# Performance work log

Hardware: AMD Instinct MI355X
Metric: run time of the kernel (lower is better)

The kernel has to match this reference:

```python
import jax, jax.numpy as jnp
import numpy as np

B, C, H, W = 32, 1536, 32, 32
M_CLUSTERS, L_DIM, G_DIM = 64, 128, 256
SINKHORN_ITERS = 3
EPS = 1e-12

def setup_inputs() -> dict:
    key = jax.random.key(0)
    ks = jax.random.split(key, 16)
    s = lambda i, shape, scale=0.02: jax.random.normal(ks[i], shape, jnp.float32) * scale
    return {
        'x': jax.random.normal(ks[0], (B, C, H, W), jnp.float32),
        't': jax.random.normal(ks[1], (B, C), jnp.float32),
        'cf_w1': s(2, (512, C)), 'cf_b1': s(3, (512,)),
        'cf_w2': s(4, (L_DIM, 512)), 'cf_b2': s(5, (L_DIM,)),
        'sc_w1': s(6, (512, C)), 'sc_b1': s(7, (512,)),
        'sc_w2': s(8, (M_CLUSTERS, 512)), 'sc_b2': s(9, (M_CLUSTERS,)),
        'tk_w1': s(10, (512, C)), 'tk_b1': s(11, (512,)),
        'tk_w2': s(12, (G_DIM, 512)), 'tk_b2': s(13, (G_DIM,)),
        'dust_bin': jnp.array(1.0, jnp.float32),
    }

def _l2norm(v, axis):
    n = jnp.sqrt(jnp.sum(v * v, axis=axis, keepdims=True))
    return v / jnp.maximum(n, EPS)

def _log_optimal_transport(scores, alpha, iters):
    # scores: [B, m, n]; append dustbin row, run log-space Sinkhorn
    b, m, n = scores.shape
    norm = -jnp.log(jnp.float32(m + n))
    bins = jnp.broadcast_to(alpha, (b, 1, n))
    Z0 = jnp.concatenate([scores, bins], axis=1)             # [B, m+1, n]
    log_mu = jnp.concatenate([jnp.full((m,), norm, jnp.float32),
                              jnp.log(jnp.float32(n - m))[None] + norm])  # [m+1]
    log_nu = jnp.full((n,), norm, jnp.float32)               # [n]
    u = jnp.zeros((b, m + 1), jnp.float32)
    v = jnp.zeros((b, n), jnp.float32)
    for _ in range(iters):
        u = log_mu[None, :] - jax.nn.logsumexp(Z0 + v[:, None, :], axis=2)
        v = log_nu[None, :] - jax.nn.logsumexp(Z0 + u[:, :, None], axis=1)
    return Z0 + u[:, :, None] + v[:, None, :] - norm

def reference(x, t, cf_w1, cf_b1, cf_w2, cf_b2, sc_w1, sc_b1, sc_w2, sc_b2,
              tk_w1, tk_b1, tk_w2, tk_b2, dust_bin):
    b = x.shape[0]
    xf = x.reshape(b, x.shape[1], -1)                        # [B, C, HW]
    # cluster_features: 1x1 conv stack -> [B, l, HW]
    h = jax.nn.relu(jnp.einsum('oc,bcn->bon', cf_w1, xf) + cf_b1[None, :, None])
    f = jnp.einsum('oc,bcn->bon', cf_w2, h) + cf_b2[None, :, None]
    # score: 1x1 conv stack -> [B, m, HW]
    h = jax.nn.relu(jnp.einsum('oc,bcn->bon', sc_w1, xf) + sc_b1[None, :, None])
    p = jnp.einsum('oc,bcn->bon', sc_w2, h) + sc_b2[None, :, None]
    # token_features: MLP -> [B, g]
    tk = jax.nn.relu(t @ tk_w1.T + tk_b1) @ tk_w2.T + tk_b2
    # Sinkhorn OT assignment, drop dustbin row
    p = jnp.exp(_log_optimal_transport(p, dust_bin, SINKHORN_ITERS))[:, :-1, :]  # [B, m, HW]
    # fused VLAD aggregation (avoids the repeat-materialized tensors)
    agg = jnp.einsum('bln,bmn->blm', f, p)                   # [B, l, m]
    agg = _l2norm(agg, axis=1).reshape(b, -1)                # [B, l*m]
    v = jnp.concatenate([_l2norm(tk, axis=-1), agg], axis=-1)
    return _l2norm(v, axis=-1)
```

## Files before the change

### kernel.cpp

```cpp
#include <hip/hip_runtime.h>
#include <hip/hip_bf16.h>
#include <math.h>

typedef unsigned short u16;
typedef __attribute__((ext_vector_type(8))) short short8;
typedef __attribute__((ext_vector_type(4))) float floatx4;

#define DEVINL __device__ __forceinline__

DEVINL float bf2f(u16 u) { union { unsigned int i; float f; } v; v.i = ((unsigned int)u) << 16; return v.f; }
DEVINL u16 f2bf(float f) {
  union { unsigned int i; float f; } v; v.f = f;
  unsigned int i = v.i;
  unsigned int r = (i + 0x7fffu + ((i >> 16) & 1u)) >> 16;
  return (u16)r;
}

__global__ __launch_bounds__(256) void k_prep(
    const float* __restrict__ cf_w1, u16* __restrict__ wc1,
    const float* __restrict__ sc_w1, u16* __restrict__ ws1,
    const float* __restrict__ cf_w2, u16* __restrict__ wc2,
    const float* __restrict__ sc_w2, u16* __restrict__ ws2p,
    const float* __restrict__ sc_b2, float* __restrict__ scb2p) {
  int i = blockIdx.x * 256 + threadIdx.x;
  int job = blockIdx.y;
  if (job == 4) {
    if (i < 128) scb2p[i] = (i < 64) ? sc_b2[i] : 0.f;
    return;
  }
  const float* src = (job == 0) ? cf_w1 : (job == 1) ? sc_w1 : (job == 2) ? cf_w2 : sc_w2;
  u16* dst = (job == 0) ? wc1 : (job == 1) ? ws1 : (job == 2) ? wc2 : ws2p;
  int n4 = (job <= 1) ? 196608 : 16384;
  if (i >= n4) return;
  ushort4 o = {0, 0, 0, 0};
  if (job != 3 || (i >> 7) < 64) {
    float4 v = ((const float4*)src)[i];
    o.x = f2bf(v.x); o.y = f2bf(v.y); o.z = f2bf(v.z); o.w = f2bf(v.w);
  }
  ((ushort4*)dst)[i] = o;
}

__global__ __launch_bounds__(256) void k_transpose(const float* __restrict__ x,
                                                   u16* __restrict__ xT,
                                                   int nC, int nN) {
  __shared__ u16 tile[64 * 65];
  int b = blockIdx.z;
  int c0 = blockIdx.y * 64, n0 = blockIdx.x * 64;
  const float* xb = x + ((long)b * nC + c0) * nN + n0;
  u16* xTb = xT + ((long)b * nN + n0) * nC + c0;
  int tid = threadIdx.x;
#pragma unroll
  for (int p = 0; p < 2; ++p) {
    int u = tid + p * 256;
    int r = u >> 3, nc = (u & 7) * 8;
    const float4* srcp = (const float4*)(xb + (long)r * nN + nc);
    float4 v0 = srcp[0], v1 = srcp[1];
    int base = r * 65 + nc;
    tile[base + 0] = f2bf(v0.x); tile[base + 1] = f2bf(v0.y);
    tile[base + 2] = f2bf(v0.z); tile[base + 3] = f2bf(v0.w);
    tile[base + 4] = f2bf(v1.x); tile[base + 5] = f2bf(v1.y);
    tile[base + 6] = f2bf(v1.z); tile[base + 7] = f2bf(v1.w);
  }
  __syncthreads();
#pragma unroll
  for (int p = 0; p < 2; ++p) {
    int u = tid + p * 256;
    int nr = u >> 3, cc = (u & 7) * 8;
    __align__(16) u16 tmp[8];
#pragma unroll
    for (int j = 0; j < 8; ++j) tmp[j] = tile[(cc + j) * 65 + nr];
    *(uint4*)(xTb + (long)nr * nC + cc) = *(uint4*)(tmp);
  }
}

template <bool OUT_F32, int BIAS_MODE, bool RELU>
__global__ __launch_bounds__(256) void k_gemm64(
    const u16* __restrict__ A, int lda, long aBS,
    const u16* __restrict__ B1, const u16* __restrict__ B2, int nSplit,
    int ldb, long bBS,
    void* __restrict__ Out, int ldo, long oBS,
    const float* __restrict__ bias1, const float* __restrict__ bias2,
    int M, int N, int K) {
  __shared__ __align__(16) u16 As[128 * 64];
  __shared__ __align__(16) u16 Bs[128 * 64];
  int bz = blockIdx.z;
  int m0 = blockIdx.x * 128, n0 = blockIdx.y * 128;
  const u16* Ablk = A + (long)bz * aBS + (long)m0 * lda;
  const u16* Bblk =
      ((n0 < nSplit) ? (B1 + (long)n0 * ldb) : (B2 + (long)(n0 - nSplit) * ldb)) +
      (long)bz * bBS;
  int tid = threadIdx.x;
  int lane = tid & 63;
  int lane16 = lane & 15, quad = lane >> 4;
  int wid = tid >> 6;
  int wm = wid >> 1, wn = wid & 1;

  int rIn = lane >> 3;
  int kkSw = ((lane & 7) ^ rIn) * 8;

  floatx4 acc[4][4];
#pragma unroll
  for (int i = 0; i < 4; ++i)
#pragma unroll
    for (int j = 0; j < 4; ++j) acc[i][j] = (floatx4){0.f, 0.f, 0.f, 0.f};

  for (int k0 = 0; k0 < K; k0 += 64) {
    __syncthreads();
#pragma unroll
    for (int h = 0; h < 4; ++h) {
      int ch = wid * 4 + h;
      int r = ch * 8 + rIn;
      const u16* srcA = Ablk + (long)r * lda + k0 + kkSw;
      __builtin_amdgcn_global_load_lds(
          (const __attribute__((address_space(1))) void*)srcA,
          (__attribute__((address_space(3))) void*)&As[ch * 512], 16, 0, 0);
      const u16* srcB = Bblk + (long)r * ldb + k0 + kkSw;
      __builtin_amdgcn_global_load_lds(
          (const __attribute__((address_space(1))) void*)srcB,
          (__attribute__((address_space(3))) void*)&Bs[ch * 512], 16, 0, 0);
    }
    __syncthreads();
#pragma unroll
    for (int h2 = 0; h2 < 2; ++h2) {
      short8 af[4], bfr[4];
#pragma unroll
      for (int t = 0; t < 4; ++t) {
        int ra = wm * 64 + t * 16 + lane16;
        af[t] = *(const short8*)&As[ra * 64 + (((h2 * 4 + quad) ^ (ra & 7)) * 8)];
      }
#pragma unroll
      for (int t = 0; t < 4; ++t) {
        int rb = wn * 64 + t * 16 + lane16;
        bfr[t] = *(const short8*)&Bs[rb * 64 + (((h2 * 4 + quad) ^ (rb & 7)) * 8)];
      }
#pragma unroll
      for (int i = 0; i < 4; ++i)
#pragma unroll
        for (int j = 0; j < 4; ++j)
          acc[i][j] = __builtin_amdgcn_mfma_f32_16x16x32_bf16(af[i], bfr[j],
                                                              acc[i][j], 0, 0, 0);
    }
  }

  const float* bcolPtr = bias1;
  int bofs = 0;
  if (BIAS_MODE == 2 && n0 >= nSplit) { bcolPtr = bias2; bofs = nSplit; }
#pragma unroll
  for (int i = 0; i < 4; ++i) {
    int rowb = m0 + wm * 64 + i * 16 + quad * 4;
#pragma unroll
    for (int j = 0; j < 4; ++j) {
      int col = n0 + wn * 64 + j * 16 + lane16;
      float bc = 0.f;
      if (BIAS_MODE == 2) bc = bcolPtr[col - bofs];
#pragma unroll
      for (int r = 0; r < 4; ++r) {
        int row = rowb + r;
        float v = acc[i][j][r];
        if (BIAS_MODE == 2) v += bc;
        if (BIAS_MODE == 1) v += bias1[row];
        if (RELU) v = fmaxf(v, 0.f);
        if (OUT_F32)
          ((float*)Out)[(long)bz * oBS + (long)row * ldo + col] = v;
        else
          ((u16*)Out)[(long)bz * oBS + (long)row * ldo + col] = f2bf(v);
      }
    }
  }
}

__global__ __launch_bounds__(256) void k_k2dual(
    const u16* __restrict__ wA, const u16* __restrict__ wB,
    const u16* __restrict__ hT, u16* __restrict__ fOut, u16* __restrict__ sOut,
    const float* __restrict__ bA, const float* __restrict__ bB) {
  __shared__ __align__(16) u16 As[128 * 64];
  __shared__ __align__(16) u16 Bs[128 * 64];
  int sel = blockIdx.y, bz = blockIdx.z;
  const u16* A = sel ? wB : wA;
  const u16* Bbase = hT + (long)bz * 1048576 + (sel ? 512 : 0);
  u16* Out = (sel ? sOut : fOut) + (long)bz * 131072;
  const float* bias = sel ? bB : bA;
  int n0 = blockIdx.x * 128;
  int tid = threadIdx.x;
  int lane = tid & 63;
  int lane16 = lane & 15, quad = lane >> 4;
  int wid = tid >> 6;
  int wm = wid >> 1, wn = wid & 1;
  int rIn = lane >> 3;
  int kkSw = ((lane & 7) ^ rIn) * 8;

  floatx4 acc[4][4];
#pragma unroll
  for (int i = 0; i < 4; ++i)
#pragma unroll
    for (int j = 0; j < 4; ++j) acc[i][j] = (floatx4){0.f, 0.f, 0.f, 0.f};

  for (int k0 = 0; k0 < 512; k0 += 64) {
    __syncthreads();
#pragma unroll
    for (int h = 0; h < 4; ++h) {
      int ch = wid * 4 + h;
      int r = ch * 8 + rIn;
      const u16* srcA = A + (long)r * 512 + k0 + kkSw;
      __builtin_amdgcn_global_load_lds(
          (const __attribute__((address_space(1))) void*)srcA,
          (__attribute__((address_space(3))) void*)&As[ch * 512], 16, 0, 0);
      const u16* srcB = Bbase + (long)(n0 + r) * 1024 + k0 + kkSw;
      __builtin_amdgcn_global_load_lds(
          (const __attribute__((address_space(1))) void*)srcB,
          (__attribute__((address_space(3))) void*)&Bs[ch * 512], 16, 0, 0);
    }
    __syncthreads();
#pragma unroll
    for (int h2 = 0; h2 < 2; ++h2) {
      short8 af[4], bfr[4];
#pragma unroll
      for (int t = 0; t < 4; ++t) {
        int ra = wm * 64 + t * 16 + lane16;
        af[t] = *(const short8*)&As[ra * 64 + (((h2 * 4 + quad) ^ (ra & 7)) * 8)];
      }
#pragma unroll
      for (int t = 0; t < 4; ++t) {
        int rb = wn * 64 + t * 16 + lane16;
        bfr[t] = *(const short8*)&Bs[rb * 64 + (((h2 * 4 + quad) ^ (rb & 7)) * 8)];
      }
#pragma unroll
      for (int i = 0; i < 4; ++i)
#pragma unroll
        for (int j = 0; j < 4; ++j)
          acc[i][j] = __builtin_amdgcn_mfma_f32_16x16x32_bf16(af[i], bfr[j],
                                                              acc[i][j], 0, 0, 0);
    }
  }
#pragma unroll
  for (int i = 0; i < 4; ++i) {
    int rowb = wm * 64 + i * 16 + quad * 4;
#pragma unroll
    for (int j = 0; j < 4; ++j) {
      int col = n0 + wn * 64 + j * 16 + lane16;
#pragma unroll
      for (int r = 0; r < 4; ++r) {
        int row = rowb + r;
        Out[(long)row * 1024 + col] = f2bf(acc[i][j][r] + bias[row]);
      }
    }
  }
}

__global__ __launch_bounds__(1024) void k_sinkhorn(
    const u16* __restrict__ S, const float* __restrict__ alphaPtr,
    float lmu, float lmu_bin, float lnu, float norm, u16* __restrict__ P) {
  __shared__ float u_[65];
  __shared__ float v_[1024];
  int b = blockIdx.x, tid = threadIdx.x;
  const u16* Sb = S + (long)b * 131072;
  float alpha = *alphaPtr;
  v_[tid] = 0.f;
  __syncthreads();
  int wid = tid >> 6, lane = tid & 63;
  for (int it = 0; it < 3; ++it) {
    for (int i = wid; i < 65; i += 16) {
      float vals[16];
      float mx = -3.4e38f;
#pragma unroll
      for (int s = 0; s < 16; ++s) {
        int j = lane + s * 64;
        float z = (i < 64 ? bf2f(Sb[i * 1024 + j]) : alpha) + v_[j];
        vals[s] = z;
        mx = fmaxf(mx, z);
      }
#pragma unroll
      for (int off = 32; off > 0; off >>= 1) mx = fmaxf(mx, __shfl_xor(mx, off));
      float sum = 0.f;
#pragma unroll
      for (int s = 0; s < 16; ++s) sum += __expf(vals[s] - mx);
#pragma unroll
      for (int off = 32; off > 0; off >>= 1) sum += __shfl_xor(sum, off);
      if (lane == 0) u_[i] = (i < 64 ? lmu : lmu_bin) - (mx + __logf(sum));
    }
    __syncthreads();
    {
      float mx = alpha + u_[64];
#pragma unroll 8
      for (int i = 0; i < 64; ++i)
        mx = fmaxf(mx, bf2f(Sb[i * 1024 + tid]) + u_[i]);
      float sum = __expf(alpha + u_[64] - mx);
#pragma unroll 8
      for (int i = 0; i < 64; ++i)
        sum += __expf(bf2f(Sb[i * 1024 + tid]) + u_[i] - mx);
      v_[tid] = lnu - (mx + __logf(sum));
    }
    __syncthreads();
  }
  float vj = v_[tid];
  u16* Pb = P + (long)b * 65536;
#pragma unroll 8
  for (int i = 0; i < 64; ++i) {
    float z = bf2f(Sb[i * 1024 + tid]) + u_[i] + vj - norm;
    Pb[i * 1024 + tid] = f2bf(__expf(fminf(z, 1.0f)));
  }
}

__global__ __launch_bounds__(256) void k_agg(const u16* __restrict__ f,
                                             const u16* __restrict__ P,
                                             float* __restrict__ aggP) {
  __shared__ __align__(16) u16 Fs[128 * 32];
  __shared__ __align__(16) u16 Ps[64 * 32];
  int bz = blockIdx.z, kc = blockIdx.x;
  const u16* Fb = f + (long)bz * 128 * 1024;
  const u16* Pb = P + (long)bz * 64 * 1024;
  int tid = threadIdx.x, wid = tid >> 6, lane = tid & 63;
  int lane16 = lane & 15, quad = lane >> 4;
  int rA0 = lane >> 2, kk = (lane & 3) * 8;

  floatx4 acc[2][4];
#pragma unroll
  for (int i = 0; i < 2; ++i)
#pragma unroll
    for (int j = 0; j < 4; ++j) acc[i][j] = (floatx4){0.f, 0.f, 0.f, 0.f};

  for (int k0 = kc * 256; k0 < kc * 256 + 256; k0 += 32) {
    __syncthreads();
#pragma unroll
    for (int h = 0; h < 2; ++h) {
      int ch = wid * 2 + h;
      int r = ch * 16 + rA0;
      const u16* srcF = Fb + (long)r * 1024 + k0 + kk;
      __builtin_amdgcn_global_load_lds(
          (const __attribute__((address_space(1))) void*)srcF,
          (__attribute__((address_space(3))) void*)&Fs[ch * 512], 16, 0, 0);
    }
    {
      int r = wid * 16 + rA0;
      const u16* srcP = Pb + (long)r * 1024 + k0 + kk;
      __builtin_amdgcn_global_load_lds(
          (const __attribute__((address_space(1))) void*)srcP,
          (__attribute__((address_space(3))) void*)&Ps[wid * 512], 16, 0, 0);
    }
    __syncthreads();
    short8 af[2], bfr[4];
#pragma unroll
    for (int t = 0; t < 2; ++t)
      af[t] = *(const short8*)&Fs[(wid * 32 + t * 16 + lane16) * 32 + quad * 8];
#pragma unroll
    for (int j = 0; j < 4; ++j)
      bfr[j] = *(const short8*)&Ps[(j * 16 + lane16) * 32 + quad * 8];
#pragma unroll
    for (int i = 0; i < 2; ++i)
#pragma unroll
      for (int j = 0; j < 4; ++j)
        acc[i][j] = __builtin_amdgcn_mfma_f32_16x16x32_bf16(af[i], bfr[j],
                                                            acc[i][j], 0, 0, 0);
  }
  float* ab = aggP + ((long)kc * 32 + bz) * 8192;
#pragma unroll
  for (int i = 0; i < 2; ++i)
#pragma unroll
    for (int j = 0; j < 4; ++j)
#pragma unroll
      for (int r = 0; r < 4; ++r) {
        int row = wid * 32 + i * 16 + quad * 4 + r;
        int col = j * 16 + lane16;
        ab[row * 64 + col] = acc[i][j][r];
      }
}

DEVINL float waveSum(float x) {
#pragma unroll
  for (int off = 32; off > 0; off >>= 1) x += __shfl_xor(x, off);
  return x;
}

__global__ __launch_bounds__(256) void k_mlp1(const float* __restrict__ t,
                                              const float* __restrict__ w1,
                                              const float* __restrict__ b1,
                                              float* __restrict__ h1) {
  __shared__ float tl[1536];
  int b = blockIdx.y, og = blockIdx.x;
  int tid = threadIdx.x, wid = tid >> 6, lane = tid & 63;
  for (int i = tid; i < 1536; i += 256) tl[i] = t[b * 1536 + i];
  __syncthreads();
#pragma unroll 4
  for (int oi = 0; oi < 16; ++oi) {
    int o = og * 64 + wid * 16 + oi;
    const float* wr = w1 + (long)o * 1536;
    float acc = 0.f;
#pragma unroll
    for (int s = 0; s < 24; ++s) { int c = lane + s * 64; acc += tl[c] * wr[c]; }
    acc = waveSum(acc);
    if (lane == 0) h1[b * 512 + o] = fmaxf(acc + b1[o], 0.f);
  }
}

__global__ __launch_bounds__(256) void k_mlp2(const float* __restrict__ h1,
                                              const float* __restrict__ w2,
                                              const float* __restrict__ b2,
                                              float* __restrict__ tk) {
  __shared__ float hl[512];
  int b = blockIdx.y, og = blockIdx.x;
  int tid = threadIdx.x, wid = tid >> 6, lane = tid & 63;
  for (int i = tid; i < 512; i += 256) hl[i] = h1[b * 512 + i];
  __syncthreads();
#pragma unroll 4
  for (int oi = 0; oi < 16; ++oi) {
    int o = og * 64 + wid * 16 + oi;
    const float* wr = w2 + (long)o * 512;
    float acc = 0.f;
#pragma unroll
    for (int s = 0; s < 8; ++s) { int c = lane + s * 64; acc += hl[c] * wr[c]; }
    acc = waveSum(acc);
    if (lane == 0) tk[b * 256 + o] = acc + b2[o];
  }
}

DEVINL float blockSum256(float x, float* red) {
#pragma unroll
  for (int off = 32; off > 0; off >>= 1) x += __shfl_xor(x, off);
  int wid = threadIdx.x >> 6;
  __syncthreads();
  if ((threadIdx.x & 63) == 0) red[wid] = x;
  __syncthreads();
  return red[0] + red[1] + red[2] + red[3];
}

__global__ __launch_bounds__(256) void k_norms(const float* __restrict__ tk,
                                               const float* __restrict__ aggP,
                                               float* __restrict__ out) {
  __shared__ float asum[8192];
  __shared__ float cn[64];
  __shared__ float red[4];
  int b = blockIdx.x, tid = threadIdx.x;
  const float* a0 = aggP + (long)b * 8192;
  for (int idx = tid; idx < 8192; idx += 256)
    asum[idx] = a0[idx] + a0[32 * 8192 + idx] + a0[64 * 8192 + idx] +
                a0[96 * 8192 + idx];
  __syncthreads();
  float tkv = tk[b * 256 + tid];
  float tss = blockSum256(tkv * tkv, red);
  float tn = fmaxf(sqrtf(tss), 1e-12f);
  if (tid < 64) {
    float s = 0.f;
    for (int l = 0; l < 128; ++l) { float a = asum[l * 64 + tid]; s += a * a; }
    cn[tid] = fmaxf(sqrtf(s), 1e-12f);
  }
  __syncthreads();
  float gs = (tkv / tn) * (tkv / tn);
  for (int idx = tid; idx < 8192; idx += 256) {
    float a = asum[idx] / cn[idx & 63];
    gs += a * a;
  }
  float G = blockSum256(gs, red);
  float inv = 1.f / fmaxf(sqrtf(G), 1e-12f);
  float* ob = out + (long)b * 8448;
  ob[tid] = tkv / tn * inv;
  for (int idx = tid; idx < 8192; idx += 256)
    ob[256 + idx] = asum[idx] / cn[idx & 63] * inv;
}

extern "C" void kernel_launch(void* const* d_in, const int* in_sizes, int n_in,
                              void* d_out, int out_size, void* d_ws,
                              size_t ws_size, hipStream_t stream) {
  const float* x = (const float*)d_in[0];
  const float* t = (const float*)d_in[1];
  const float* cf_w1 = (const float*)d_in[2];
  const float* cf_b1 = (const float*)d_in[3];
  const float* cf_w2 = (const float*)d_in[4];
  const float* cf_b2 = (const float*)d_in[5];
  const float* sc_w1 = (const float*)d_in[6];
  const float* sc_b1 = (const float*)d_in[7];
  const float* sc_w2 = (const float*)d_in[8];
  const float* sc_b2 = (const float*)d_in[9];
  const float* tk_w1 = (const float*)d_in[10];
  const float* tk_b1 = (const float*)d_in[11];
  const float* tk_w2 = (const float*)d_in[12];
  const float* tk_b2 = (const float*)d_in[13];
  const float* dust = (const float*)d_in[14];
  float* out = (float*)d_out;

  char* ws = (char*)d_ws;
  size_t off = 0;
  u16* wc1 = (u16*)(ws + off); off += (size_t)512 * 1536 * 2;
  u16* ws1 = (u16*)(ws + off); off += (size_t)512 * 1536 * 2;
  u16* wc2 = (u16*)(ws + off); off += (size_t)128 * 512 * 2;
  u16* ws2p = (u16*)(ws + off); off += (size_t)128 * 512 * 2;
  float* scb2p = (float*)(ws + off); off += (size_t)128 * 4;
  u16* f = (u16*)(ws + off);   off += (size_t)32 * 128 * 1024 * 2;
  u16* scr = (u16*)(ws + off); off += (size_t)32 * 128 * 1024 * 2;
  u16* P = (u16*)(ws + off);   off += (size_t)32 * 64 * 1024 * 2;
  float* aggP = (float*)(ws + off); off += (size_t)4 * 32 * 128 * 64 * 4;
  float* h1ws = (float*)(ws + off); off += (size_t)32 * 512 * 4;
  float* tkws = (float*)(ws + off); off += (size_t)32 * 256 * 4;
  size_t fixed = off;
  size_t perB = (size_t)1024 * 1536 * 2 + (size_t)1024 * 1024 * 2;
  int c = 1;
  const int cands[6] = {32, 16, 8, 4, 2, 1};
  for (int k = 0; k < 6; ++k)
    if (fixed + (size_t)cands[k] * perB <= ws_size) { c = cands[k]; break; }
  u16* xT = (u16*)(ws + fixed);
  u16* hT = (u16*)(ws + fixed + (size_t)c * 1024 * 1536 * 2);

  k_prep<<<dim3(768, 5), 256, 0, stream>>>(cf_w1, wc1, sc_w1, ws1, cf_w2, wc2,
                                           sc_w2, ws2p, sc_b2, scb2p);

  k_mlp1<<<dim3(8, 32), 256, 0, stream>>>(t, tk_w1, tk_b1, h1ws);
  k_mlp2<<<dim3(4, 32), 256, 0, stream>>>(h1ws, tk_w2, tk_b2, tkws);

  float norm = -logf(1088.f);
  float lmu = norm;
  float lmu_bin = logf(960.f) + norm;
  float lnu = norm;

  for (int cb = 0; cb < 32; cb += c) {
    k_transpose<<<dim3(16, 24, c), 256, 0, stream>>>(
        x + (size_t)cb * 1536 * 1024, xT, 1536, 1024);
    k_gemm64<false, 2, true><<<dim3(8, 8, c), 256, 0, stream>>>(
        xT, 1536, (long)1024 * 1536,
        wc1, ws1, 512, 1536, 0,
        hT, 1024, (long)1024 * 1024,
        cf_b1, sc_b1, 1024, 1024, 1536);
    k_k2dual<<<dim3(8, 2, c), 256, 0, stream>>>(
        wc2, ws2p, hT, f + (size_t)cb * 131072, scr + (size_t)cb * 131072,
        cf_b2, scb2p);
  }
  k_sinkhorn<<<32, 1024, 0, stream>>>(scr, dust, lmu, lmu_bin, lnu, norm, P);
  k_agg<<<dim3(4, 1, 32), 256, 0, stream>>>(f, P, aggP);
  k_norms<<<32, 256, 0, stream>>>(tkws, aggP, out);
}
```

Before: 598.2 us.

## Precompute load offsets in GEMM loops and keep Sinkhorn scores in registers

The GEMM and aggregation kernels now compute their per-thread byte offsets once and advance base pointers each K step, with the K trip count made a template constant. This cuts the address arithmetic inside the load loops. The Sinkhorn kernel loads each thread's 64 score values into registers once instead of re-reading global memory every iteration. Row max and sum are now reduced across all 16 waves through shared memory, which adds syncs and raises register pressure.

Result: slower. 678.3 us (+13.4%).

```diff
diff --git a/kernel.cpp b/kernel.cpp
--- a/kernel.cpp
+++ b/kernel.cpp
@@ -7,6 +7,8 @@
 typedef __attribute__((ext_vector_type(4))) float floatx4;
 
 #define DEVINL __device__ __forceinline__
+#define AS1 __attribute__((address_space(1)))
+#define AS3 __attribute__((address_space(3)))
 
 DEVINL float bf2f(u16 u) { union { unsigned int i; float f; } v; v.i = ((unsigned int)u) << 16; return v.f; }
 DEVINL u16 f2bf(float f) {
@@ -73,22 +75,21 @@
   }
 }
 
-template <bool OUT_F32, int BIAS_MODE, bool RELU>
+template <int KT, bool OUT_F32, int BIAS_MODE, bool RELU>
 __global__ __launch_bounds__(256) void k_gemm64(
     const u16* __restrict__ A, int lda, long aBS,
     const u16* __restrict__ B1, const u16* __restrict__ B2, int nSplit,
     int ldb, long bBS,
     void* __restrict__ Out, int ldo, long oBS,
-    const float* __restrict__ bias1, const float* __restrict__ bias2,
-    int M, int N, int K) {
+    const float* __restrict__ bias1, const float* __restrict__ bias2) {
   __shared__ __align__(16) u16 As[128 * 64];
   __shared__ __align__(16) u16 Bs[128 * 64];
   int bz = blockIdx.z;
   int m0 = blockIdx.x * 128, n0 = blockIdx.y * 128;
-  const u16* Ablk = A + (long)bz * aBS + (long)m0 * lda;
-  const u16* Bblk =
+  const char* pA = (const char*)(A + (long)bz * aBS + (long)m0 * lda);
+  const char* pB = (const char*)(
       ((n0 < nSplit) ? (B1 + (long)n0 * ldb) : (B2 + (long)(n0 - nSplit) * ldb)) +
-      (long)bz * bBS;
+      (long)bz * bBS);
   int tid = threadIdx.x;
   int lane = tid & 63;
   int lane16 = lane & 15, quad = lane >> 4;
@@ -98,27 +99,31 @@
   int rIn = lane >> 3;
   int kkSw = ((lane & 7) ^ rIn) * 8;
 
+  int voA[4], voB[4];
+#pragma unroll
+  for (int h = 0; h < 4; ++h) {
+    int r = (wid * 4 + h) * 8 + rIn;
+    voA[h] = (r * lda + kkSw) * 2;
+    voB[h] = (r * ldb + kkSw) * 2;
+  }
+
   floatx4 acc[4][4];
 #pragma unroll
   for (int i = 0; i < 4; ++i)
 #pragma unroll
     for (int j = 0; j < 4; ++j) acc[i][j] = (floatx4){0.f, 0.f, 0.f, 0.f};
 
-  for (int k0 = 0; k0 < K; k0 += 64) {
+  for (int kt = 0; kt < KT; ++kt) {
     __syncthreads();
 #pragma unroll
     for (int h = 0; h < 4; ++h) {
-      int ch = wid * 4 + h;
-      int r = ch * 8 + rIn;
-      const u16* srcA = Ablk + (long)r * lda + k0 + kkSw;
-      __builtin_amdgcn_global_load_lds(
-          (const __attribute__((address_space(1))) void*)srcA,
-          (__attribute__((address_space(3))) void*)&As[ch * 512], 16, 0, 0);
-      const u16* srcB = Bblk + (long)r * ldb + k0 + kkSw;
-      __builtin_amdgcn_global_load_lds(
-          (const __attribute__((address_space(1))) void*)srcB,
-          (__attribute__((address_space(3))) void*)&Bs[ch * 512], 16, 0, 0);
-    }
+      __builtin_amdgcn_global_load_lds((const AS1 void*)(pA + voA[h]),
+                                       (AS3 void*)&As[(wid * 4 + h) * 512], 16, 0, 0);
+      __builtin_amdgcn_global_load_lds((const AS1 void*)(pB + voB[h]),
+                                       (AS3 void*)&Bs[(wid * 4 + h) * 512], 16, 0, 0);
+    }
+    pA += 128;
+    pB += 128;
     __syncthreads();
 #pragma unroll
     for (int h2 = 0; h2 < 2; ++h2) {
@@ -176,11 +181,12 @@
   __shared__ __align__(16) u16 As[128 * 64];
   __shared__ __align__(16) u16 Bs[128 * 64];
   int sel = blockIdx.y, bz = blockIdx.z;
-  const u16* A = sel ? wB : wA;
-  const u16* Bbase = hT + (long)bz * 1048576 + (sel ? 512 : 0);
+  int n0 = blockIdx.x * 128;
+  const char* pA = (const char*)(sel ? wB : wA);
+  const char* pB = (const char*)(hT + (long)bz * 1048576 + (sel ? 512 : 0) +
+                                 (long)n0 * 1024);
   u16* Out = (sel ? sOut : fOut) + (long)bz * 131072;
   const float* bias = sel ? bB : bA;
-  int n0 = blockIdx.x * 128;
   int tid = threadIdx.x;
   int lane = tid & 63;
   int lane16 = lane & 15, quad = lane >> 4;
@@ -189,27 +195,31 @@
   int rIn = lane >> 3;
   int kkSw = ((lane & 7) ^ rIn) * 8;
 
+  int voA[4], voB[4];
+#pragma unroll
+  for (int h = 0; h < 4; ++h) {
+    int r = (wid * 4 + h) * 8 + rIn;
+    voA[h] = (r * 512 + kkSw) * 2;
+    voB[h] = (r * 1024 + kkSw) * 2;
+  }
+
   floatx4 acc[4][4];
 #pragma unroll
   for (int i = 0; i < 4; ++i)
 #pragma unroll
     for (int j = 0; j < 4; ++j) acc[i][j] = (floatx4){0.f, 0.f, 0.f, 0.f};
 
-  for (int k0 = 0; k0 < 512; k0 += 64) {
+  for (int kt = 0; kt < 8; ++kt) {
     __syncthreads();
 #pragma unroll
     for (int h = 0; h < 4; ++h) {
-      int ch = wid * 4 + h;
-      int r = ch * 8 + rIn;
-      const u16* srcA = A + (long)r * 512 + k0 + kkSw;
-      __builtin_amdgcn_global_load_lds(
-          (const __attribute__((address_space(1))) void*)srcA,
-          (__attribute__((address_space(3))) void*)&As[ch * 512], 16, 0, 0);
-      const u16* srcB = Bbase + (long)(n0 + r) * 1024 + k0 + kkSw;
-      __builtin_amdgcn_global_load_lds(
-          (const __attribute__((address_space(1))) void*)srcB,
-          (__attribute__((address_space(3))) void*)&Bs[ch * 512], 16, 0, 0);
-    }
+      __builtin_amdgcn_global_load_lds((const AS1 void*)(pA + voA[h]),
+                                       (AS3 void*)&As[(wid * 4 + h) * 512], 16, 0, 0);
+      __builtin_amdgcn_global_load_lds((const AS1 void*)(pB + voB[h]),
+                                       (AS3 void*)&Bs[(wid * 4 + h) * 512], 16, 0, 0);
+    }
+    pA += 128;
+    pB += 128;
     __syncthreads();
 #pragma unroll
     for (int h2 = 0; h2 < 2; ++h2) {
@@ -247,56 +257,74 @@
   }
 }
 
+DEVINL float waveMax(float x) {
+#pragma unroll
+  for (int off = 32; off > 0; off >>= 1) x = fmaxf(x, __shfl_xor(x, off));
+  return x;
+}
+DEVINL float waveSum(float x) {
+#pragma unroll
+  for (int off = 32; off > 0; off >>= 1) x += __shfl_xor(x, off);
+  return x;
+}
+
 __global__ __launch_bounds__(1024) void k_sinkhorn(
     const u16* __restrict__ S, const float* __restrict__ alphaPtr,
     float lmu, float lmu_bin, float lnu, float norm, u16* __restrict__ P) {
+  __shared__ float wred[65][17];
+  __shared__ float rowm[65];
   __shared__ float u_[65];
-  __shared__ float v_[1024];
   int b = blockIdx.x, tid = threadIdx.x;
+  int wid = tid >> 6, lane = tid & 63;
   const u16* Sb = S + (long)b * 131072;
   float alpha = *alphaPtr;
-  v_[tid] = 0.f;
-  __syncthreads();
-  int wid = tid >> 6, lane = tid & 63;
+  float s[64];
+#pragma unroll
+  for (int i = 0; i < 64; ++i) s[i] = bf2f(Sb[i * 1024 + tid]);
+  float v = 0.f;
   for (int it = 0; it < 3; ++it) {
-    for (int i = wid; i < 65; i += 16) {
-      float vals[16];
-      float mx = -3.4e38f;
-#pragma unroll
-      for (int s = 0; s < 16; ++s) {
-        int j = lane + s * 64;
-        float z = (i < 64 ? bf2f(Sb[i * 1024 + j]) : alpha) + v_[j];
-        vals[s] = z;
-        mx = fmaxf(mx, z);
-      }
-#pragma unroll
-      for (int off = 32; off > 0; off >>= 1) mx = fmaxf(mx, __shfl_xor(mx, off));
-      float sum = 0.f;
-#pragma unroll
-      for (int s = 0; s < 16; ++s) sum += __expf(vals[s] - mx);
-#pragma unroll
-      for (int off = 32; off > 0; off >>= 1) sum += __shfl_xor(sum, off);
-      if (lane == 0) u_[i] = (i < 64 ? lmu : lmu_bin) - (mx + __logf(sum));
-    }
-    __syncthreads();
-    {
-      float mx = alpha + u_[64];
-#pragma unroll 8
-      for (int i = 0; i < 64; ++i)
-        mx = fmaxf(mx, bf2f(Sb[i * 1024 + tid]) + u_[i]);
-      float sum = __expf(alpha + u_[64] - mx);
-#pragma unroll 8
-      for (int i = 0; i < 64; ++i)
-        sum += __expf(bf2f(Sb[i * 1024 + tid]) + u_[i] - mx);
-      v_[tid] = lnu - (mx + __logf(sum));
-    }
-    __syncthreads();
-  }
-  float vj = v_[tid];
+#pragma unroll
+    for (int i = 0; i < 65; ++i) {
+      float z = (i < 64 ? s[i] : alpha) + v;
+      float m = waveMax(z);
+      if (lane == 0) wred[i][wid] = m;
+    }
+    __syncthreads();
+    if (tid < 65) {
+      float m = wred[tid][0];
+#pragma unroll
+      for (int w = 1; w < 16; ++w) m = fmaxf(m, wred[tid][w]);
+      rowm[tid] = m;
+    }
+    __syncthreads();
+#pragma unroll
+    for (int i = 0; i < 65; ++i) {
+      float z = (i < 64 ? s[i] : alpha) + v;
+      float e = __expf(z - rowm[i]);
+      float sm = waveSum(e);
+      if (lane == 0) wred[i][wid] = sm;
+    }
+    __syncthreads();
+    if (tid < 65) {
+      float sm = 0.f;
+#pragma unroll
+      for (int w = 0; w < 16; ++w) sm += wred[tid][w];
+      u_[tid] = (tid < 64 ? lmu : lmu_bin) - (rowm[tid] + __logf(sm));
+    }
+    __syncthreads();
+    float mx = alpha + u_[64];
+#pragma unroll
+    for (int i = 0; i < 64; ++i) mx = fmaxf(mx, s[i] + u_[i]);
+    float sum = __expf(alpha + u_[64] - mx);
+#pragma unroll
+    for (int i = 0; i < 64; ++i) sum += __expf(s[i] + u_[i] - mx);
+    v = lnu - (mx + __logf(sum));
+    __syncthreads();
+  }
   u16* Pb = P + (long)b * 65536;
-#pragma unroll 8
+#pragma unroll
   for (int i = 0; i < 64; ++i) {
-    float z = bf2f(Sb[i * 1024 + tid]) + u_[i] + vj - norm;
+    float z = s[i] + u_[i] + v - norm;
     Pb[i * 1024 + tid] = f2bf(__expf(fminf(z, 1.0f)));
   }
 }
@@ -307,11 +335,16 @@
   __shared__ __align__(16) u16 Fs[128 * 32];
   __shared__ __align__(16) u16 Ps[64 * 32];
   int bz = blockIdx.z, kc = blockIdx.x;
-  const u16* Fb = f + (long)bz * 128 * 1024;
-  const u16* Pb = P + (long)bz * 64 * 1024;
   int tid = threadIdx.x, wid = tid >> 6, lane = tid & 63;
   int lane16 = lane & 15, quad = lane >> 4;
   int rA0 = lane >> 2, kk = (lane & 3) * 8;
+  const char* pF = (const char*)(f + (long)bz * 131072 + kc * 256);
+  const char* pP = (const char*)(P + (long)bz * 65536 + kc * 256);
+  int voF[2];
+#pragma unroll
+  for (int h = 0; h < 2; ++h)
+    voF[h] = (((wid * 2 + h) * 16 + rA0) * 1024 + kk) * 2;
+  int voP = ((wid * 16 + rA0) * 1024 + kk) * 2;
 
   floatx4 acc[2][4];
 #pragma unroll
@@ -319,24 +352,16 @@
 #pragma unroll
     for (int j = 0; j < 4; ++j) acc[i][j] = (floatx4){0.f, 0.f, 0.f, 0.f};
 
-  for (int k0 = kc * 256; k0 < kc * 256 + 256; k0 += 32) {
-    __syncthreads();
-#pragma unroll
-    for (int h = 0; h < 2; ++h) {
-      int ch = wid * 2 + h;
-      int r = ch * 16 + rA0;
-      const u16* srcF = Fb + (long)r * 1024 + k0 + kk;
-      __builtin_amdgcn_global_load_lds(
-          (const __attribute__((address_space(1))) void*)srcF,
-          (__attribute__((address_space(3))) void*)&Fs[ch * 512], 16, 0, 0);
-    }
-    {
-      int r = wid * 16 + rA0;
-      const u16* srcP = Pb + (long)r * 1024 + k0 + kk;
-      __builtin_amdgcn_global_load_lds(
-          (const __attribute__((address_space(1))) void*)srcP,
-          (__attribute__((address_space(3))) void*)&Ps[wid * 512], 16, 0, 0);
-    }
+  for (int kt = 0; kt < 8; ++kt) {
+    __syncthreads();
+#pragma unroll
+    for (int h = 0; h < 2; ++h)
+      __builtin_amdgcn_global_load_lds((const AS1 void*)(pF + voF[h]),
+                                       (AS3 void*)&Fs[(wid * 2 + h) * 512], 16, 0, 0);
+    __builtin_amdgcn_global_load_lds((const AS1 void*)(pP + voP),
+                                     (AS3 void*)&Ps[wid * 512], 16, 0, 0);
+    pF += 64;
+    pP += 64;
     __syncthreads();
     short8 af[2], bfr[4];
 #pragma unroll
@@ -363,12 +388,6 @@
         int col = j * 16 + lane16;
         ab[row * 64 + col] = acc[i][j][r];
       }
-}
-
-DEVINL float waveSum(float x) {
-#pragma unroll
-  for (int off = 32; off > 0; off >>= 1) x += __shfl_xor(x, off);
-  return x;
 }
 
 __global__ __launch_bounds__(256) void k_mlp1(const float* __restrict__ t,
@@ -513,11 +532,11 @@
   for (int cb = 0; cb < 32; cb += c) {
     k_transpose<<<dim3(16, 24, c), 256, 0, stream>>>(
         x + (size_t)cb * 1536 * 1024, xT, 1536, 1024);
-    k_gemm64<false, 2, true><<<dim3(8, 8, c), 256, 0, stream>>>(
+    k_gemm64<24, false, 2, true><<<dim3(8, 8, c), 256, 0, stream>>>(
         xT, 1536, (long)1024 * 1536,
         wc1, ws1, 512, 1536, 0,
         hT, 1024, (long)1024 * 1024,
-        cf_b1, sc_b1, 1024, 1024, 1536);
+        cf_b1, sc_b1);
     k_k2dual<<<dim3(8, 2, c), 256, 0, stream>>>(
         wc2, ws2p, hT, f + (size_t)cb * 131072, scr + (size_t)cb * 131072,
         cf_b2, scb2p);
```
